# Performance work log

Measured on AMD Instinct MI355X. Metric: run time of the kernel, lower is better.

The kernel has to match this reference:

```python
import jax, jax.numpy as jnp
import numpy as np

B, N, P, PL = 8, 16, 128, 16
D, DS, DTR, DFF, EL = 128, 16, 8, 256, 2


def setup_inputs() -> dict:
    key = jax.random.key(0)
    ks = jax.random.split(key, 16)
    g = lambda i, shape, s=0.02: jax.random.normal(ks[i], shape, dtype=jnp.float32) * s
    A_init = jnp.broadcast_to(jnp.log(jnp.arange(1, DS + 1, dtype=jnp.float32)), (EL, 2, D, DS))
    return dict(
        x=jax.random.normal(ks[0], (B, N, P, PL), dtype=jnp.float32),
        view=jax.random.normal(ks[1], (B, 1, D), dtype=jnp.float32),
        wp_w=g(2, (D, PL)), wp_b=jnp.zeros((D,), jnp.float32),
        m_in_w=g(3, (EL, 2, 2 * D, D)),
        m_conv_w=g(4, (EL, 2, D, 2), 0.5), m_conv_b=jnp.zeros((EL, 2, D), jnp.float32),
        m_xproj_w=g(5, (EL, 2, DTR + 2 * DS, D)),
        m_dt_w=g(6, (EL, 2, D, DTR), 0.1), m_dt_b=jnp.full((EL, 2, D), -4.6, jnp.float32),
        m_Alog=jnp.array(A_init),
        m_D=jnp.ones((EL, 2, D), jnp.float32),
        m_out_w=g(7, (EL, 2, D, D)),
        ffn_w1=g(8, (EL, DFF, D)), ffn_b1=jnp.zeros((EL, DFF), jnp.float32),
        ffn_w2=g(9, (EL, D, DFF)), ffn_b2=jnp.zeros((EL, D), jnp.float32),
        ln1_g=jnp.ones((EL, D), jnp.float32), ln1_b=jnp.zeros((EL, D), jnp.float32),
        ln2_g=jnp.ones((EL, D), jnp.float32), ln2_b=jnp.zeros((EL, D), jnp.float32),
        lnf_g=jnp.ones((D,), jnp.float32), lnf_b=jnp.zeros((D,), jnp.float32),
    )


def _ln(x, g, b, eps=1e-5):
    m = x.mean(-1, keepdims=True)
    v = x.var(-1, keepdims=True)
    return (x - m) * jax.lax.rsqrt(v + eps) * g + b


def _mamba(u, in_w, conv_w, conv_b, xproj_w, dt_w, dt_b, A_log, Dp, out_w):
    # u: [b, L, d]; d_inner == d_model (expand=1), causal depthwise conv with kernel 2
    dtr, ds = dt_w.shape[1], A_log.shape[1]
    xz = u @ in_w.T                               # [b, L, 2d]
    xc, z = jnp.split(xz, 2, axis=-1)
    xp = jnp.pad(xc, ((0, 0), (1, 0), (0, 0)))    # left-pad (d_conv-1 = 1)
    xc = xp[:, :-1, :] * conv_w[:, 0] + xp[:, 1:, :] * conv_w[:, 1] + conv_b
    xc = jax.nn.silu(xc)
    dbc = xc @ xproj_w.T                          # [b, L, dtr + 2*ds]
    dt = jax.nn.softplus(dbc[..., :dtr] @ dt_w.T + dt_b)   # [b, L, d]
    Bm = dbc[..., dtr:dtr + ds]                   # [b, L, n]
    Cm = dbc[..., dtr + ds:]                      # [b, L, n]
    A = -jnp.exp(A_log)                           # [d, n]
    dA = jnp.exp(dt[..., None] * A)               # [b, L, d, n]
    dBx = dt[..., None] * Bm[:, :, None, :] * xc[..., None]  # [b, L, d, n]

    def step(h, ab):
        a, bx = ab
        h = a * h + bx
        return h, h

    h0 = jnp.zeros((u.shape[0], dt.shape[-1], ds), u.dtype)
    _, hs = jax.lax.scan(step, h0, (jnp.moveaxis(dA, 1, 0), jnp.moveaxis(dBx, 1, 0)))
    y = jnp.einsum('lbdn,bln->bld', hs, Cm)       # [b, L, d]
    y = y + xc * Dp
    y = y * jax.nn.silu(z)
    return y @ out_w.T


def _layer(u, pf, pr, w1, b1, w2, b2, g1, be1, g2, be2):
    fwd = _mamba(u, *pf)
    rev = _mamba(u[:, ::-1], *pr)[:, ::-1]
    u = u + fwd + rev
    xr = _ln(u, g1, be1)
    y = jax.nn.relu(xr @ w1.T + b1) @ w2.T + b2   # 1x1 conv FFN == pointwise linear
    return _ln(xr + y, g2, be2)


def reference(x, view, wp_w, wp_b, m_in_w, m_conv_w, m_conv_b, m_xproj_w, m_dt_w,
              m_dt_b, m_Alog, m_D, m_out_w, ffn_w1, ffn_b1, ffn_w2, ffn_b2,
              ln1_g, ln1_b, ln2_g, ln2_b, lnf_g, lnf_b):
    b, n, p, _ = x.shape
    u = x @ wp_w.T + wp_b                         # [b, n, p, d]
    d = u.shape[-1]
    u = u.reshape(b, n * p, d)
    u = jnp.concatenate([u, view], axis=1)        # [b, n*p+1, d]
    for l in range(m_in_w.shape[0]):
        pf = (m_in_w[l, 0], m_conv_w[l, 0], m_conv_b[l, 0], m_xproj_w[l, 0],
              m_dt_w[l, 0], m_dt_b[l, 0], m_Alog[l, 0], m_D[l, 0], m_out_w[l, 0])
        pr = (m_in_w[l, 1], m_conv_w[l, 1], m_conv_b[l, 1], m_xproj_w[l, 1],
              m_dt_w[l, 1], m_dt_b[l, 1], m_Alog[l, 1], m_D[l, 1], m_out_w[l, 1])
        u = _layer(u, pf, pr, ffn_w1[l], ffn_b1[l], ffn_w2[l], ffn_b2[l],
                   ln1_g[l], ln1_b[l], ln2_g[l], ln2_b[l])
    u = _ln(u, lnf_g, lnf_b)
    z = u[:, :-1, :].reshape(b, n, p, d)
    return z.transpose(0, 1, 3, 2)                # [b, n, d, p]
```

## Files before the change

kernel.cpp:

```cpp
#include <hip/hip_runtime.h>
#include <hip/hip_bf16.h>
#include <math.h>

#define DEV __device__ __forceinline__

constexpr int B  = 8,  N = 16, P = 128, PL = 16;
constexpr int D  = 128, DS = 16, DTR = 8, DFF = 256, EL = 2;
constexpr int L  = N * P + 1;
constexpr int BL = B * L;
constexpr int CT = 32;
constexpr int NC = (L + CT - 1) / CT;
constexpr int MT64  = (BL + 63) / 64;
constexpr int MT32  = (BL + 31) / 32;
constexpr int KS = 136;
constexpr int HS = 264;

using bf16x8 = __attribute__((ext_vector_type(8))) __bf16;
using f32x4  = __attribute__((ext_vector_type(4))) float;

DEV float sigmoidf_(float x) { return 1.0f / (1.0f + __expf(-x)); }

DEV void pow_tree(float r, float* pw) {
  float r2 = r * r;
  float r3 = r2 * r;
  float r4 = r2 * r2;
  float r8 = r4 * r4;
  float r12 = r8 * r4;
  pw[0] = r;       pw[1] = r2;      pw[2] = r3;      pw[3] = r4;
  pw[4] = r4 * r;  pw[5] = r4 * r2; pw[6] = r4 * r3; pw[7] = r8;
  pw[8] = r8 * r;  pw[9] = r8 * r2; pw[10] = r8 * r3; pw[11] = r12;
  pw[12] = r12 * r; pw[13] = r12 * r2; pw[14] = r12 * r3; pw[15] = r12 * r4;
}

DEV bool an_is_linear(const float* An) {
  bool ok = true;
#pragma unroll
  for (int n = 0; n < DS; ++n)
    ok = ok && (fabsf(An[n] + (float)(n + 1)) < 1e-3f * (n + 1));
  return ok;
}

__global__ __launch_bounds__(256) void k_prep(
    const float* __restrict__ in_w, const float* __restrict__ conv_w,
    const float* __restrict__ xproj, const float* __restrict__ out_w,
    const float* __restrict__ w1, const float* __restrict__ w2,
    __bf16* __restrict__ weff, __bf16* __restrict__ xpw_bf,
    __bf16* __restrict__ outw_bf, __bf16* __restrict__ w1_bf,
    __bf16* __restrict__ w2_bf)
{
  int g = blockIdx.x * 256 + threadIdx.x;
  if (g < 262144) {
    int l = g >> 17;
    int r = g & 131071;
    int dir = r >> 16;
    int r2 = r & 65535;
    int col = r2 >> 8;
    int kk = r2 & 255;
    int chunk = kk >> 7, k = kk & 127;
    int ld = l * 2 + dir;
    float v;
    if (col < 128) {
      v = in_w[((size_t)ld * 256 + col) * 128 + k] *
          conv_w[((size_t)ld * 128 + col) * 2 + chunk];
    } else {
      v = chunk ? in_w[((size_t)ld * 256 + col) * 128 + k] : 0.f;
    }
    weff[((size_t)ld * 256 + col) * 256 + chunk * 128 + k] = (__bf16)v;
    return;
  }
  g -= 262144;
  if (g < 20480) { xpw_bf[g] = (__bf16)xproj[g]; return; }
  g -= 20480;
  if (g < 65536) {
    int k = g & 127; int q = g >> 7; int n = q & 127; int q2 = q >> 7;
    int dir = q2 & 1; int l = q2 >> 1;
    outw_bf[((size_t)(l * 128 + n)) * 256 + dir * 128 + k] = (__bf16)out_w[g];
    return;
  }
  g -= 65536;
  if (g < 65536) { w1_bf[g] = (__bf16)w1[g]; return; }
  g -= 65536;
  if (g < 65536) { w2_bf[g] = (__bf16)w2[g]; return; }
}

__global__ __launch_bounds__(256) void k_embed(
    const float* __restrict__ x, const float* __restrict__ view,
    const float* __restrict__ wp_w, const float* __restrict__ wp_b,
    float* __restrict__ U, __bf16* __restrict__ Ubf)
{
  int g = blockIdx.x * 256 + threadIdx.x;
  if (g >= BL * D) return;
  int d = g & (D - 1);
  int row = g >> 7;
  int b = row / L, t = row % L;
  float acc;
  if (t < N * P) {
    const float* xr = x + ((size_t)b * N * P + t) * PL;
    acc = wp_b[d];
#pragma unroll
    for (int k = 0; k < PL; ++k) acc += xr[k] * wp_w[d * PL + k];
  } else {
    acc = view[b * D + d];
  }
  U[(size_t)row * D + d] = acc;
  Ubf[(size_t)row * D + d] = (__bf16)acc;
}

__global__ __launch_bounds__(256) void k_front(
    const __bf16* __restrict__ Ubf, const __bf16* __restrict__ Weff,
    const float* __restrict__ conv_b_l, const __bf16* __restrict__ xpw,
    const float* __restrict__ dt_w_l, const float* __restrict__ dt_b_l,
    __bf16* __restrict__ XCCbf, __bf16* __restrict__ Zbf,
    float* __restrict__ BCb, __bf16* __restrict__ DTbf)
{
  __shared__ short As[64 * KS];
  __shared__ short Ws[64 * KS];
  __shared__ float dbs[64][9];
  int bx = blockIdx.x;
  int rdir = bx / MT64;
  int tile = bx % MT64;
  bool isx = (blockIdx.y == 0);
  int tid = threadIdx.x;
  int m0 = tile * 64;
  const __bf16* Wb = Weff + (size_t)rdir * 256 * 256;
  int wave = tid >> 6, lane = tid & 63, lm = lane & 15, lq = lane >> 4;
  int rr0 = tid >> 4, gcol = tid & 15;

  int aoff[4];
  unsigned vmask = 0, smask = 0;
  int shif = rdir ? 128 : -128;
#pragma unroll
  for (int i = 0; i < 4; ++i) {
    int rr = rr0 + 16 * i;
    int m = m0 + rr;
    aoff[i] = 0;
    if (m < BL) {
      int b = m / L, s = m - b * L;
      int idx1 = rdir ? (L - 1 - s) : s;
      aoff[i] = (b * L + idx1) * 128 + gcol * 8;
      vmask |= 1u << i;
      if (s >= 1) smask |= 1u << i;
    }
  }

  f32x4 zero4 = {0.f, 0.f, 0.f, 0.f};
  f32x4 acc[8];
#pragma unroll
  for (int c = 0; c < 8; ++c) acc[c] = zero4;

  int kc0 = isx ? 0 : 1;
  int colx = isx ? 0 : 128;
  for (int kc = kc0; kc < 2; ++kc) {
    if (kc != kc0) __syncthreads();
#pragma unroll
    for (int i = 0; i < 4; ++i) {
      int rr = rr0 + 16 * i;
      int4 v = make_int4(0, 0, 0, 0);
      bool ok = (vmask >> i) & 1;
      if (kc == 0) ok = ok && ((smask >> i) & 1);
      if (ok) v = *(const int4*)(Ubf + aoff[i] + (kc == 0 ? shif : 0));
      *(int4*)&As[rr * KS + gcol * 8] = v;
    }
    for (int ch = 0; ch < 2; ++ch) {
      if (ch) __syncthreads();
#pragma unroll
      for (int i = 0; i < 4; ++i) {
        int rr = rr0 + 16 * i;
        int4 v = *(const int4*)(Wb + (size_t)(colx + ch * 64 + rr) * 256 + kc * 128 + gcol * 8);
        *(int4*)&Ws[rr * KS + gcol * 8] = v;
      }
      __syncthreads();
      for (int ks = 0; ks < 128; ks += 32) {
        bf16x8 af = *(const bf16x8*)&As[(wave * 16 + lm) * KS + ks + lq * 8];
#pragma unroll
        for (int c = 0; c < 4; ++c) {
          bf16x8 bfr = *(const bf16x8*)&Ws[(c * 16 + lm) * KS + ks + lq * 8];
          acc[ch * 4 + c] = __builtin_amdgcn_mfma_f32_16x16x32_bf16(af, bfr, acc[ch * 4 + c], 0, 0, 0);
        }
      }
    }
  }

  if (!isx) {
#pragma unroll
    for (int cg = 0; cg < 8; ++cg) {
      int col = cg * 16 + lm;
#pragma unroll
      for (int e = 0; e < 4; ++e) {
        int m = m0 + wave * 16 + lq * 4 + e;
        if (m < BL)
          Zbf[((size_t)rdir * BL + m) * 128 + col] = (__bf16)acc[cg][e];
      }
    }
    return;
  }

  __syncthreads();
#pragma unroll
  for (int cg = 0; cg < 8; ++cg) {
    int col = cg * 16 + lm;
    float cb = conv_b_l[rdir * 128 + col];
#pragma unroll
    for (int e = 0; e < 4; ++e) {
      int rl = wave * 16 + lq * 4 + e;
      int m = m0 + rl;
      float v = acc[cg][e] + cb;
      float o = v * sigmoidf_(v);
      __bf16 ob = (__bf16)o;
      if (m < BL) XCCbf[((size_t)rdir * BL + m) * 128 + col] = ob;
      As[rl * KS + col] = (short)__builtin_bit_cast(unsigned short, ob);
    }
  }
#pragma unroll
  for (int i = 0; i < 3; ++i) {
    int rr = rr0 + 16 * i;
    int4 v = make_int4(0, 0, 0, 0);
    if (rr < 40) v = *(const int4*)(xpw + ((size_t)rdir * 40 + rr) * 128 + gcol * 8);
    *(int4*)&Ws[rr * KS + gcol * 8] = v;
  }
  __syncthreads();
  f32x4 acc2[3];
#pragma unroll
  for (int c = 0; c < 3; ++c) acc2[c] = zero4;
  for (int ks = 0; ks < 128; ks += 32) {
    bf16x8 af = *(const bf16x8*)&As[(wave * 16 + lm) * KS + ks + lq * 8];
#pragma unroll
    for (int c = 0; c < 3; ++c) {
      bf16x8 bfr = *(const bf16x8*)&Ws[(c * 16 + lm) * KS + ks + lq * 8];
      acc2[c] = __builtin_amdgcn_mfma_f32_16x16x32_bf16(af, bfr, acc2[c], 0, 0, 0);
    }
  }
#pragma unroll
  for (int c = 0; c < 3; ++c) {
    int col = c * 16 + lm;
#pragma unroll
    for (int e = 0; e < 4; ++e) {
      int rl = wave * 16 + lq * 4 + e;
      int m = m0 + rl;
      float v = acc2[c][e];
      if (col < DTR) dbs[rl][col] = v;
      else if (col < DTR + 2 * DS && m < BL)
        BCb[((size_t)rdir * BL + m) * 32 + (col - DTR)] = v;
    }
  }
  __syncthreads();
  {
    int dloc = tid & 127;
    int rpar = tid >> 7;
    const float* dw = dt_w_l + ((size_t)rdir * 128 + dloc) * 8;
    float dwr[8];
#pragma unroll
    for (int j = 0; j < 8; ++j) dwr[j] = dw[j];
    float db = dt_b_l[rdir * 128 + dloc];
    for (int rr = rpar; rr < 64; rr += 2) {
      int m = m0 + rr;
      if (m >= BL) break;
      float a = db;
#pragma unroll
      for (int j = 0; j < 8; ++j) a = fmaf(dbs[rr][j], dwr[j], a);
      float dtv = (a > 20.f) ? a : log1pf(__expf(a));
      DTbf[((size_t)rdir * BL + m) * 128 + dloc] = (__bf16)dtv;
    }
  }
}

__global__ __launch_bounds__(128) void k_scanA(
    const __bf16* __restrict__ DTbf, const __bf16* __restrict__ XCCbf,
    const float* __restrict__ BCb, const float* __restrict__ Alog_l,
    float* __restrict__ HC, float* __restrict__ DTS)
{
  __shared__ float Bs[CT][DS];
  __shared__ __bf16 DTs[CT][128];
  __shared__ __bf16 XCs[CT][128];
  __shared__ float HT[128][DS + 1];
  int blk = blockIdx.x;
  int c  = blk % NC;
  int rb = blk / NC;
  int rdir = rb / B;
  int d = threadIdx.x;
  int s0 = c * CT;
  int cn = min(CT, L - s0);
  size_t rowbase = (size_t)rb * L + s0;
  for (int q = d; q < cn * DS; q += 128)
    Bs[q >> 4][q & 15] = BCb[(rowbase + (q >> 4)) * 32 + (q & 15)];
  for (int q = d; q < cn * 16; q += 128) {
    int row = q >> 4, c8 = (q & 15) * 8;
    *(int4*)&DTs[row][c8] = *(const int4*)(DTbf + (rowbase + row) * D + c8);
    *(int4*)&XCs[row][c8] = *(const int4*)(XCCbf + (rowbase + row) * D + c8);
  }
  float An[DS];
  const float* Ab = Alog_l + (size_t)rdir * D * DS + (size_t)d * DS;
#pragma unroll
  for (int n = 0; n < DS; ++n) An[n] = -__expf(Ab[n]);
  bool fast = an_is_linear(An);
  __syncthreads();
  float h[DS];
#pragma unroll
  for (int n = 0; n < DS; ++n) h[n] = 0.f;
  float dts = 0.f;
  if (fast) {
    for (int ss = 0; ss < cn; ++ss) {
      float dt = (float)DTs[ss][d];
      float xc = (float)XCs[ss][d];
      dts += dt;
      float e = dt * xc;
      float pw[DS];
      pow_tree(__expf(-dt), pw);
#pragma unroll
      for (int n = 0; n < DS; ++n)
        h[n] = fmaf(pw[n], h[n], e * Bs[ss][n]);
    }
  } else {
    for (int ss = 0; ss < cn; ++ss) {
      float dt = (float)DTs[ss][d];
      float xc = (float)XCs[ss][d];
      dts += dt;
      float e = dt * xc;
#pragma unroll
      for (int n = 0; n < DS; ++n)
        h[n] = __expf(dt * An[n]) * h[n] + e * Bs[ss][n];
    }
  }
  DTS[(size_t)blk * D + d] = dts;
#pragma unroll
  for (int n = 0; n < DS; ++n) HT[d][n] = h[n];
  __syncthreads();
  for (int q = d; q < D * DS; q += 128) {
    int n = q >> 7, dd = q & 127;
    HC[((size_t)blk * DS + n) * D + dd] = HT[dd][n];
  }
}

__global__ __launch_bounds__(128) void k_scanB(
    const float* __restrict__ HC, const float* __restrict__ DTS,
    const float* __restrict__ Alog_l, float* __restrict__ HIN)
{
  int rb = blockIdx.x >> 4;
  int n  = blockIdx.x & 15;
  int rdir = rb / B;
  int d = threadIdx.x;
  float An_v = -__expf(Alog_l[((size_t)rdir * D + d) * DS + n]);
  float hc[8], dts[8];
#pragma unroll
  for (int k = 0; k < 8; ++k) {
    int cc = (k < NC) ? k : NC - 1;
    hc[k]  = HC[((size_t)(rb * NC + cc) * DS + n) * D + d];
    dts[k] = DTS[((size_t)(rb * NC + cc)) * D + d];
  }
  float h = 0.f;
  for (int c = 0; c < NC; c += 8) {
#pragma unroll
    for (int k = 0; k < 8; ++k) {
      int cc = c + k;
      if (cc >= NC) break;
      HIN[((size_t)(rb * NC + cc) * DS + n) * D + d] = h;
      h = __expf(dts[k] * An_v) * h + hc[k];
      int cp = cc + 8 < NC ? cc + 8 : NC - 1;
      hc[k]  = HC[((size_t)(rb * NC + cp) * DS + n) * D + d];
      dts[k] = DTS[((size_t)(rb * NC + cp)) * D + d];
    }
  }
}

__global__ __launch_bounds__(128) void k_scanC(
    const __bf16* __restrict__ DTbf, const __bf16* __restrict__ XCCbf,
    const float* __restrict__ BCb, const __bf16* __restrict__ Zbf,
    const float* __restrict__ HIN, const float* __restrict__ Alog_l,
    const float* __restrict__ Dp_l, __bf16* __restrict__ YMbf)
{
  __shared__ float Bsm[CT][DS];
  __shared__ float Csm[CT][DS];
  __shared__ __bf16 DTs[CT][128];
  __shared__ __bf16 XCs[CT][128];
  __shared__ __bf16 Zs[CT][128];
  int blk = blockIdx.x;
  int c  = blk % NC;
  int rb = blk / NC;
  int rdir = rb / B;
  int b = rb % B;
  int d = threadIdx.x;
  int s0 = c * CT;
  int cn = min(CT, L - s0);
  size_t rowbase = (size_t)rb * L + s0;
  for (int q = d; q < cn * 2 * DS; q += 128) {
    int ss = q >> 5, j = q & 31;
    float vv = BCb[(rowbase + ss) * 32 + j];
    if (j < DS) Bsm[ss][j] = vv; else Csm[ss][j - DS] = vv;
  }
  for (int q = d; q < cn * 16; q += 128) {
    int row = q >> 4, c8 = (q & 15) * 8;
    *(int4*)&DTs[row][c8] = *(const int4*)(DTbf + (rowbase + row) * D + c8);
    *(int4*)&XCs[row][c8] = *(const int4*)(XCCbf + (rowbase + row) * D + c8);
    *(int4*)&Zs[row][c8]  = *(const int4*)(Zbf + (rowbase + row) * D + c8);
  }
  float An[DS];
  const float* Ab = Alog_l + (size_t)rdir * D * DS + (size_t)d * DS;
#pragma unroll
  for (int n = 0; n < DS; ++n) An[n] = -__expf(Ab[n]);
  bool fast = an_is_linear(An);
  float h[DS];
#pragma unroll
  for (int n = 0; n < DS; ++n)
    h[n] = HIN[((size_t)blk * DS + n) * D + d];
  float Dpv = Dp_l[rdir * D + d];
  __syncthreads();
  if (fast) {
    for (int ss = 0; ss < cn; ++ss) {
      float dt = (float)DTs[ss][d];
      float xc = (float)XCs[ss][d];
      float z  = (float)Zs[ss][d];
      float e = dt * xc;
      float pw[DS];
      pow_tree(__expf(-dt), pw);
      float y = xc * Dpv;
#pragma unroll
      for (int n = 0; n < DS; ++n) {
        h[n] = fmaf(pw[n], h[n], e * Bsm[ss][n]);
        y = fmaf(h[n], Csm[ss][n], y);
      }
      y *= z * sigmoidf_(z);
      int s = s0 + ss;
      int tt = rdir ? (L - 1 - s) : s;
      YMbf[((size_t)b * L + tt) * 256 + rdir * 128 + d] = (__bf16)y;
    }
  } else {
    for (int ss = 0; ss < cn; ++ss) {
      float dt = (float)DTs[ss][d];
      float xc = (float)XCs[ss][d];
      float z  = (float)Zs[ss][d];
      float e = dt * xc;
      float y = xc * Dpv;
#pragma unroll
      for (int n = 0; n < DS; ++n) {
        h[n] = __expf(dt * An[n]) * h[n] + e * Bsm[ss][n];
        y = fmaf(h[n], Csm[ss][n], y);
      }
      y *= z * sigmoidf_(z);
      int s = s0 + ss;
      int tt = rdir ? (L - 1 - s) : s;
      YMbf[((size_t)b * L + tt) * 256 + rdir * 128 + d] = (__bf16)y;
    }
  }
}

__global__ __launch_bounds__(256) void k_tail(
    const __bf16* __restrict__ YMbf, const __bf16* __restrict__ Wout,
    const float* __restrict__ g1, const float* __restrict__ be1,
    const __bf16* __restrict__ w1bf, const float* __restrict__ b1,
    const __bf16* __restrict__ w2bf, const float* __restrict__ b2,
    const float* __restrict__ g2, const float* __restrict__ be2,
    float* __restrict__ U, __bf16* __restrict__ Ubf,
    int last, const float* __restrict__ lnfg, const float* __restrict__ lnfb,
    float* __restrict__ outp)
{
  __shared__ short AX[32 * KS];
  __shared__ short HB[32 * HS];
  __shared__ short Ws[128 * KS];
  __shared__ float red[2][32][2];
  int m0 = blockIdx.x * 32;
  int tid = threadIdx.x;
  int wave = tid >> 6, lane = tid & 63, lm = lane & 15, lq = lane >> 4;
  int wm = wave >> 1, wn = wave & 1;
  f32x4 zero4 = {0.f, 0.f, 0.f, 0.f};

  f32x4 acc[4];
#pragma unroll
  for (int c = 0; c < 4; ++c) acc[c] = zero4;
  for (int kc = 0; kc < 2; ++kc) {
    if (kc) __syncthreads();
    for (int q = tid; q < 32 * 16; q += 256) {
      int rr = q >> 4, g = q & 15;
      int m = m0 + rr;
      int4 v = make_int4(0, 0, 0, 0);
      if (m < BL) v = *(const int4*)(YMbf + (size_t)m * 256 + kc * 128 + g * 8);
      *(int4*)&AX[rr * KS + g * 8] = v;
    }
    for (int q = tid; q < 128 * 16; q += 256) {
      int rr = q >> 4, g = q & 15;
      int4 v = *(const int4*)(Wout + (size_t)rr * 256 + kc * 128 + g * 8);
      *(int4*)&Ws[rr * KS + g * 8] = v;
    }
    __syncthreads();
    for (int ks = 0; ks < 128; ks += 32) {
      bf16x8 af = *(const bf16x8*)&AX[(wm * 16 + lm) * KS + ks + lq * 8];
#pragma unroll
      for (int c = 0; c < 4; ++c) {
        bf16x8 bfr = *(const bf16x8*)&Ws[(wn * 64 + c * 16 + lm) * KS + ks + lq * 8];
        acc[c] = __builtin_amdgcn_mfma_f32_16x16x32_bf16(af, bfr, acc[c], 0, 0, 0);
      }
    }
  }
  __syncthreads();

  {
    float g1c[4], be1c[4];
#pragma unroll
    for (int c = 0; c < 4; ++c) {
      int col = wn * 64 + c * 16 + lm;
      g1c[c] = g1[col]; be1c[c] = be1[col];
    }
    float os[4][4];
    float mean[4];
#pragma unroll
    for (int r = 0; r < 4; ++r) {
      int rl = wm * 16 + lq * 4 + r;
      int row = m0 + rl;
      bool valid = row < BL;
      float s = 0.f;
#pragma unroll
      for (int c = 0; c < 4; ++c) {
        int col = wn * 64 + c * 16 + lm;
        float uv = valid ? U[(size_t)row * 128 + col] : 0.f;
        os[r][c] = acc[c][r] + uv;
        s += os[r][c];
      }
#pragma unroll
      for (int mm = 1; mm < 16; mm <<= 1) s += __shfl_xor(s, mm, 64);
      if (lm == 0) red[0][rl][wn] = s;
    }
    __syncthreads();
#pragma unroll
    for (int r = 0; r < 4; ++r) {
      int rl = wm * 16 + lq * 4 + r;
      mean[r] = (red[0][rl][0] + red[0][rl][1]) * (1.f / 128.f);
      float qv = 0.f;
#pragma unroll
      for (int c = 0; c < 4; ++c) { float dv = os[r][c] - mean[r]; qv += dv * dv; }
#pragma unroll
      for (int mm = 1; mm < 16; mm <<= 1) qv += __shfl_xor(qv, mm, 64);
      if (lm == 0) red[1][rl][wn] = qv;
    }
    __syncthreads();
#pragma unroll
    for (int r = 0; r < 4; ++r) {
      int rl = wm * 16 + lq * 4 + r;
      float inv = rsqrtf((red[1][rl][0] + red[1][rl][1]) * (1.f / 128.f) + 1e-5f);
#pragma unroll
      for (int c = 0; c < 4; ++c) {
        int col = wn * 64 + c * 16 + lm;
        float o = (os[r][c] - mean[r]) * inv * g1c[c] + be1c[c];
        AX[rl * KS + col] = (short)__builtin_bit_cast(unsigned short, (__bf16)o);
      }
    }
  }

  for (int t = 0; t < 2; ++t) {
    if (t) __syncthreads();
    for (int q = tid; q < 128 * 16; q += 256) {
      int rr = q >> 4, g = q & 15;
      int4 v = *(const int4*)(w1bf + (size_t)(t * 128 + rr) * 128 + g * 8);
      *(int4*)&Ws[rr * KS + g * 8] = v;
    }
    __syncthreads();
    f32x4 a1[4];
#pragma unroll
    for (int c = 0; c < 4; ++c) a1[c] = zero4;
    for (int ks = 0; ks < 128; ks += 32) {
      bf16x8 af = *(const bf16x8*)&AX[(wm * 16 + lm) * KS + ks + lq * 8];
#pragma unroll
      for (int c = 0; c < 4; ++c) {
        bf16x8 bfr = *(const bf16x8*)&Ws[(wn * 64 + c * 16 + lm) * KS + ks + lq * 8];
        a1[c] = __builtin_amdgcn_mfma_f32_16x16x32_bf16(af, bfr, a1[c], 0, 0, 0);
      }
    }
#pragma unroll
    for (int c = 0; c < 4; ++c) {
      int col = t * 128 + wn * 64 + c * 16 + lm;
      float bb = b1[col];
#pragma unroll
      for (int e = 0; e < 4; ++e) {
        int rl = wm * 16 + lq * 4 + e;
        float hv = fmaxf(a1[c][e] + bb, 0.f);
        HB[rl * HS + col] = (short)__builtin_bit_cast(unsigned short, (__bf16)hv);
      }
    }
  }

  f32x4 a2[4];
#pragma unroll
  for (int c = 0; c < 4; ++c) a2[c] = zero4;
  for (int kc = 0; kc < 2; ++kc) {
    __syncthreads();
    for (int q = tid; q < 128 * 16; q += 256) {
      int rr = q >> 4, g = q & 15;
      int4 v = *(const int4*)(w2bf + (size_t)rr * 256 + kc * 128 + g * 8);
      *(int4*)&Ws[rr * KS + g * 8] = v;
    }
    __syncthreads();
    for (int ks = 0; ks < 128; ks += 32) {
      bf16x8 af = *(const bf16x8*)&HB[(wm * 16 + lm) * HS + kc * 128 + ks + lq * 8];
#pragma unroll
      for (int c = 0; c < 4; ++c) {
        bf16x8 bfr = *(const bf16x8*)&Ws[(wn * 64 + c * 16 + lm) * KS + ks + lq * 8];
        a2[c] = __builtin_amdgcn_mfma_f32_16x16x32_bf16(af, bfr, a2[c], 0, 0, 0);
      }
    }
  }
  __syncthreads();

  {
    float b2c[4], g2c[4], be2c[4];
#pragma unroll
    for (int c = 0; c < 4; ++c) {
      int col = wn * 64 + c * 16 + lm;
      b2c[c] = b2[col]; g2c[c] = g2[col]; be2c[c] = be2[col];
    }
    float os[4][4];
    float mean[4];
#pragma unroll
    for (int r = 0; r < 4; ++r) {
      int rl = wm * 16 + lq * 4 + r;
      float s = 0.f;
#pragma unroll
      for (int c = 0; c < 4; ++c) {
        int col = wn * 64 + c * 16 + lm;
        __bf16 xb = __builtin_bit_cast(__bf16, (unsigned short)AX[rl * KS + col]);
        os[r][c] = a2[c][r] + b2c[c] + (float)xb;
        s += os[r][c];
      }
#pragma unroll
      for (int mm = 1; mm < 16; mm <<= 1) s += __shfl_xor(s, mm, 64);
      if (lm == 0) red[0][rl][wn] = s;
    }
    __syncthreads();
#pragma unroll
    for (int r = 0; r < 4; ++r) {
      int rl = wm * 16 + lq * 4 + r;
      mean[r] = (red[0][rl][0] + red[0][rl][1]) * (1.f / 128.f);
      float qv = 0.f;
#pragma unroll
      for (int c = 0; c < 4; ++c) { float dv = os[r][c] - mean[r]; qv += dv * dv; }
#pragma unroll
      for (int mm = 1; mm < 16; mm <<= 1) qv += __shfl_xor(qv, mm, 64);
      if (lm == 0) red[1][rl][wn] = qv;
    }
    __syncthreads();
    float o[4][4];
#pragma unroll
    for (int r = 0; r < 4; ++r) {
      int rl = wm * 16 + lq * 4 + r;
      float inv = rsqrtf((red[1][rl][0] + red[1][rl][1]) * (1.f / 128.f) + 1e-5f);
#pragma unroll
      for (int c = 0; c < 4; ++c)
        o[r][c] = (os[r][c] - mean[r]) * inv * g2c[c] + be2c[c];
    }
    if (!last) {
#pragma unroll
      for (int r = 0; r < 4; ++r) {
        int rl = wm * 16 + lq * 4 + r;
        int row = m0 + rl;
        if (row < BL) {
#pragma unroll
          for (int c = 0; c < 4; ++c) {
            int col = wn * 64 + c * 16 + lm;
            U[(size_t)row * 128 + col] = o[r][c];
          }
        }
#pragma unroll
        for (int c = 0; c < 4; ++c) {
          int col = wn * 64 + c * 16 + lm;
          AX[rl * KS + col] = (short)__builtin_bit_cast(unsigned short, (__bf16)o[r][c]);
        }
      }
    } else {
      float m2[4];
#pragma unroll
      for (int r = 0; r < 4; ++r) {
        int rl = wm * 16 + lq * 4 + r;
        float s2 = 0.f;
#pragma unroll
        for (int c = 0; c < 4; ++c) s2 += o[r][c];
#pragma unroll
        for (int mm = 1; mm < 16; mm <<= 1) s2 += __shfl_xor(s2, mm, 64);
        if (lm == 0) red[0][rl][wn] = s2;
      }
      __syncthreads();
#pragma unroll
      for (int r = 0; r < 4; ++r) {
        int rl = wm * 16 + lq * 4 + r;
        m2[r] = (red[0][rl][0] + red[0][rl][1]) * (1.f / 128.f);
        float q2 = 0.f;
#pragma unroll
        for (int c = 0; c < 4; ++c) { float dv = o[r][c] - m2[r]; q2 += dv * dv; }
#pragma unroll
        for (int mm = 1; mm < 16; mm <<= 1) q2 += __shfl_xor(q2, mm, 64);
        if (lm == 0) red[1][rl][wn] = q2;
      }
      __syncthreads();
#pragma unroll
      for (int r = 0; r < 4; ++r) {
        int rl = wm * 16 + lq * 4 + r;
        int row = m0 + rl;
        float i2 = rsqrtf((red[1][rl][0] + red[1][rl][1]) * (1.f / 128.f) + 1e-5f);
        if (row < BL) {
          int bb = row / L;
          int t = row - bb * L;
          if (t < N * P) {
            int n = t >> 7, p = t & 127;
            size_t obase = (((size_t)bb * N + n) * D) * P + p;
#pragma unroll
            for (int c = 0; c < 4; ++c) {
              int col = wn * 64 + c * 16 + lm;
              float o2 = (o[r][c] - m2[r]) * i2 * lnfg[col] + lnfb[col];
              outp[obase + (size_t)col * P] = o2;
            }
          }
        }
      }
    }
  }
  if (!last) {
    __syncthreads();
    int rr0 = tid >> 4, gcol = tid & 15;
#pragma unroll
    for (int i = 0; i < 2; ++i) {
      int rr = rr0 + 16 * i;
      int m = m0 + rr;
      if (m < BL)
        *(int4*)(Ubf + (size_t)m * 128 + gcol * 8) = *(const int4*)&AX[rr * KS + gcol * 8];
    }
  }
}

extern "C" void kernel_launch(void* const* d_in, const int* in_sizes, int n_in,
                              void* d_out, int out_size, void* d_ws, size_t ws_size,
                              hipStream_t stream)
{
  (void)in_sizes; (void)n_in; (void)out_size; (void)ws_size;
  const float* x       = (const float*)d_in[0];
  const float* view    = (const float*)d_in[1];
  const float* wp_w    = (const float*)d_in[2];
  const float* wp_b    = (const float*)d_in[3];
  const float* m_in_w  = (const float*)d_in[4];
  const float* m_conv_w= (const float*)d_in[5];
  const float* m_conv_b= (const float*)d_in[6];
  const float* m_xproj = (const float*)d_in[7];
  const float* m_dt_w  = (const float*)d_in[8];
  const float* m_dt_b  = (const float*)d_in[9];
  const float* m_Alog  = (const float*)d_in[10];
  const float* m_Dp    = (const float*)d_in[11];
  const float* m_out_w = (const float*)d_in[12];
  const float* ffn_w1  = (const float*)d_in[13];
  const float* ffn_b1  = (const float*)d_in[14];
  const float* ffn_w2  = (const float*)d_in[15];
  const float* ffn_b2  = (const float*)d_in[16];
  const float* ln1_g   = (const float*)d_in[17];
  const float* ln1_b   = (const float*)d_in[18];
  const float* ln2_g   = (const float*)d_in[19];
  const float* ln2_b   = (const float*)d_in[20];
  const float* lnf_g   = (const float*)d_in[21];
  const float* lnf_b   = (const float*)d_in[22];
  float* out = (float*)d_out;

  float* W = (float*)d_ws;
  size_t off = 0;
  auto alloc = [&](size_t nfl) { float* p = W + off; off += (nfl + 3) & ~(size_t)3; return p; };
  float* U      = alloc((size_t)BL * D);
  float* Ubf_f  = alloc((size_t)BL * D / 2);
  float* XCC_f  = alloc((size_t)BL * D);
  float* Zbf_f  = alloc((size_t)BL * D);
  float* DT_f   = alloc((size_t)BL * D);
  float* BCb    = alloc((size_t)2 * BL * 2 * DS);
  float* YM_f   = alloc((size_t)BL * 256 / 2);
  float* HC     = alloc((size_t)2 * B * NC * D * DS);
  float* DTS    = alloc((size_t)2 * B * NC * D);
  float* HIN    = alloc((size_t)2 * B * NC * D * DS);
  float* weff_f = alloc(262144 / 2);
  float* xpw_f  = alloc(20480 / 2);
  float* outw_f = alloc(65536 / 2);
  float* w1_f   = alloc(65536 / 2);
  float* w2_f   = alloc(65536 / 2);

  __bf16* Ubf    = (__bf16*)Ubf_f;
  __bf16* XCCbf  = (__bf16*)XCC_f;
  __bf16* Zbf    = (__bf16*)Zbf_f;
  __bf16* DTbf   = (__bf16*)DT_f;
  __bf16* YMbf   = (__bf16*)YM_f;
  __bf16* weff   = (__bf16*)weff_f;
  __bf16* xpw_bf = (__bf16*)xpw_f;
  __bf16* outw_bf= (__bf16*)outw_f;
  __bf16* w1_bf  = (__bf16*)w1_f;
  __bf16* w2_bf  = (__bf16*)w2_f;

  k_prep<<<1872, 256, 0, stream>>>(m_in_w, m_conv_w, m_xproj, m_out_w, ffn_w1, ffn_w2,
                                   weff, xpw_bf, outw_bf, w1_bf, w2_bf);
  k_embed<<<(BL * D + 255) / 256, 256, 0, stream>>>(x, view, wp_w, wp_b, U, Ubf);

  for (int l = 0; l < EL; ++l) {
    const float* conv_b_l = m_conv_b + (size_t)l * 2 * D;
    const float* dt_w_l   = m_dt_w   + (size_t)l * 2 * D * DTR;
    const float* dt_b_l   = m_dt_b   + (size_t)l * 2 * D;
    const float* Alog_l   = m_Alog   + (size_t)l * 2 * D * DS;
    const float* Dp_l     = m_Dp     + (size_t)l * 2 * D;

    k_front <<<dim3(2 * MT64, 2), 256, 0, stream>>>(
        Ubf, weff + (size_t)l * 2 * 256 * 256, conv_b_l,
        xpw_bf + (size_t)l * 2 * 40 * 128, dt_w_l, dt_b_l,
        XCCbf, Zbf, BCb, DTbf);
    k_scanA <<<2 * B * NC, 128, 0, stream>>>(DTbf, XCCbf, BCb, Alog_l, HC, DTS);
    k_scanB <<<2 * B * 16, 128, 0, stream>>>(HC, DTS, Alog_l, HIN);
    k_scanC <<<2 * B * NC, 128, 0, stream>>>(DTbf, XCCbf, BCb, Zbf, HIN, Alog_l, Dp_l, YMbf);
    k_tail  <<<MT32, 256, 0, stream>>>(
        YMbf, outw_bf + (size_t)l * 128 * 256,
        ln1_g + l * D, ln1_b + l * D,
        w1_bf + (size_t)l * 256 * 128, ffn_b1 + l * DFF,
        w2_bf + (size_t)l * 128 * 256, ffn_b2 + l * D,
        ln2_g + l * D, ln2_b + l * D, U, Ubf,
        (l == EL - 1) ? 1 : 0, lnf_g, lnf_b, out);
  }
}
```

Measured before the change: 339.9 us.

## Merge prep/embed kernels, prefetch GEMM tiles into registers, simplify scan stores

Merges the weight-prep and embedding kernels into one launch. In k_front and k_tail, weight and activation tiles (and the residual U values) are now loaded into registers up front or one stage ahead, so global-load latency overlaps with MFMA work. The scan kernels issue all global loads before computing A and store to shared memory afterward. k_scanA writes HC straight from registers instead of transposing through a shared tile, and softplus uses __logf(1+exp) instead of log1pf. The cost is much higher register pressure, which may lower occupancy, plus slightly less accurate softplus for very negative inputs.

```diff
diff --git a/kernel.cpp b/kernel.cpp
--- a/kernel.cpp
+++ b/kernel.cpp
@@ -14,6 +14,8 @@
 constexpr int MT32  = (BL + 31) / 32;
 constexpr int KS = 136;
 constexpr int HS = 264;
+constexpr int PREP_BLOCKS  = 1872;
+constexpr int EMBED_BLOCKS = (BL * D + 255) / 256;
 
 using bf16x8 = __attribute__((ext_vector_type(8))) __bf16;
 using f32x4  = __attribute__((ext_vector_type(4))) float;
@@ -40,55 +42,55 @@
   return ok;
 }
 
-__global__ __launch_bounds__(256) void k_prep(
+__global__ __launch_bounds__(256) void k_init(
     const float* __restrict__ in_w, const float* __restrict__ conv_w,
     const float* __restrict__ xproj, const float* __restrict__ out_w,
     const float* __restrict__ w1, const float* __restrict__ w2,
     __bf16* __restrict__ weff, __bf16* __restrict__ xpw_bf,
     __bf16* __restrict__ outw_bf, __bf16* __restrict__ w1_bf,
-    __bf16* __restrict__ w2_bf)
-{
-  int g = blockIdx.x * 256 + threadIdx.x;
-  if (g < 262144) {
-    int l = g >> 17;
-    int r = g & 131071;
-    int dir = r >> 16;
-    int r2 = r & 65535;
-    int col = r2 >> 8;
-    int kk = r2 & 255;
-    int chunk = kk >> 7, k = kk & 127;
-    int ld = l * 2 + dir;
-    float v;
-    if (col < 128) {
-      v = in_w[((size_t)ld * 256 + col) * 128 + k] *
-          conv_w[((size_t)ld * 128 + col) * 2 + chunk];
-    } else {
-      v = chunk ? in_w[((size_t)ld * 256 + col) * 128 + k] : 0.f;
-    }
-    weff[((size_t)ld * 256 + col) * 256 + chunk * 128 + k] = (__bf16)v;
-    return;
-  }
-  g -= 262144;
-  if (g < 20480) { xpw_bf[g] = (__bf16)xproj[g]; return; }
-  g -= 20480;
-  if (g < 65536) {
-    int k = g & 127; int q = g >> 7; int n = q & 127; int q2 = q >> 7;
-    int dir = q2 & 1; int l = q2 >> 1;
-    outw_bf[((size_t)(l * 128 + n)) * 256 + dir * 128 + k] = (__bf16)out_w[g];
-    return;
-  }
-  g -= 65536;
-  if (g < 65536) { w1_bf[g] = (__bf16)w1[g]; return; }
-  g -= 65536;
-  if (g < 65536) { w2_bf[g] = (__bf16)w2[g]; return; }
-}
-
-__global__ __launch_bounds__(256) void k_embed(
+    __bf16* __restrict__ w2_bf,
     const float* __restrict__ x, const float* __restrict__ view,
     const float* __restrict__ wp_w, const float* __restrict__ wp_b,
     float* __restrict__ U, __bf16* __restrict__ Ubf)
 {
-  int g = blockIdx.x * 256 + threadIdx.x;
+  int bid = blockIdx.x;
+  if (bid < PREP_BLOCKS) {
+    int g = bid * 256 + threadIdx.x;
+    if (g < 262144) {
+      int l = g >> 17;
+      int r = g & 131071;
+      int dir = r >> 16;
+      int r2 = r & 65535;
+      int col = r2 >> 8;
+      int kk = r2 & 255;
+      int chunk = kk >> 7, k = kk & 127;
+      int ld = l * 2 + dir;
+      float v;
+      if (col < 128) {
+        v = in_w[((size_t)ld * 256 + col) * 128 + k] *
+            conv_w[((size_t)ld * 128 + col) * 2 + chunk];
+      } else {
+        v = chunk ? in_w[((size_t)ld * 256 + col) * 128 + k] : 0.f;
+      }
+      weff[((size_t)ld * 256 + col) * 256 + chunk * 128 + k] = (__bf16)v;
+      return;
+    }
+    g -= 262144;
+    if (g < 20480) { xpw_bf[g] = (__bf16)xproj[g]; return; }
+    g -= 20480;
+    if (g < 65536) {
+      int k = g & 127; int q = g >> 7; int n = q & 127; int q2 = q >> 7;
+      int dir = q2 & 1; int l = q2 >> 1;
+      outw_bf[((size_t)(l * 128 + n)) * 256 + dir * 128 + k] = (__bf16)out_w[g];
+      return;
+    }
+    g -= 65536;
+    if (g < 65536) { w1_bf[g] = (__bf16)w1[g]; return; }
+    g -= 65536;
+    if (g < 65536) { w2_bf[g] = (__bf16)w2[g]; return; }
+    return;
+  }
+  int g = (bid - PREP_BLOCKS) * 256 + threadIdx.x;
   if (g >= BL * D) return;
   int d = g & (D - 1);
   int row = g >> 7;
@@ -125,6 +127,24 @@
   const __bf16* Wb = Weff + (size_t)rdir * 256 * 256;
   int wave = tid >> 6, lane = tid & 63, lm = lane & 15, lq = lane >> 4;
   int rr0 = tid >> 4, gcol = tid & 15;
+  int kc0 = isx ? 0 : 1;
+  int colx = isx ? 0 : 128;
+
+  int4 wpA[4], wpB[4], wpC[4], wpD[4];
+#pragma unroll
+  for (int j = 0; j < 4; ++j)
+    wpA[j] = *(const int4*)(Wb + (size_t)(colx + 0 * 64 + rr0 + 16 * j) * 256 + kc0 * 128 + gcol * 8);
+#pragma unroll
+  for (int j = 0; j < 4; ++j)
+    wpB[j] = *(const int4*)(Wb + (size_t)(colx + 1 * 64 + rr0 + 16 * j) * 256 + kc0 * 128 + gcol * 8);
+  if (isx) {
+#pragma unroll
+    for (int j = 0; j < 4; ++j)
+      wpC[j] = *(const int4*)(Wb + (size_t)(colx + 0 * 64 + rr0 + 16 * j) * 256 + 128 + gcol * 8);
+#pragma unroll
+    for (int j = 0; j < 4; ++j)
+      wpD[j] = *(const int4*)(Wb + (size_t)(colx + 1 * 64 + rr0 + 16 * j) * 256 + 128 + gcol * 8);
+  }
 
   int aoff[4];
   unsigned vmask = 0, smask = 0;
@@ -148,26 +168,30 @@
 #pragma unroll
   for (int c = 0; c < 8; ++c) acc[c] = zero4;
 
-  int kc0 = isx ? 0 : 1;
-  int colx = isx ? 0 : 128;
   for (int kc = kc0; kc < 2; ++kc) {
     if (kc != kc0) __syncthreads();
-#pragma unroll
-    for (int i = 0; i < 4; ++i) {
-      int rr = rr0 + 16 * i;
-      int4 v = make_int4(0, 0, 0, 0);
-      bool ok = (vmask >> i) & 1;
-      if (kc == 0) ok = ok && ((smask >> i) & 1);
-      if (ok) v = *(const int4*)(Ubf + aoff[i] + (kc == 0 ? shif : 0));
-      *(int4*)&As[rr * KS + gcol * 8] = v;
+    {
+      int4 av[4];
+#pragma unroll
+      for (int i = 0; i < 4; ++i) {
+        av[i] = make_int4(0, 0, 0, 0);
+        bool ok = (vmask >> i) & 1;
+        if (kc == 0) ok = ok && ((smask >> i) & 1);
+        if (ok) av[i] = *(const int4*)(Ubf + aoff[i] + (kc == 0 ? shif : 0));
+      }
+#pragma unroll
+      for (int i = 0; i < 4; ++i)
+        *(int4*)&As[(rr0 + 16 * i) * KS + gcol * 8] = av[i];
     }
     for (int ch = 0; ch < 2; ++ch) {
       if (ch) __syncthreads();
-#pragma unroll
-      for (int i = 0; i < 4; ++i) {
-        int rr = rr0 + 16 * i;
-        int4 v = *(const int4*)(Wb + (size_t)(colx + ch * 64 + rr) * 256 + kc * 128 + gcol * 8);
-        *(int4*)&Ws[rr * KS + gcol * 8] = v;
+      {
+        int pidx = (kc - kc0) * 2 + ch;
+#pragma unroll
+        for (int i = 0; i < 4; ++i) {
+          int4 wv = (pidx == 0) ? wpA[i] : (pidx == 1) ? wpB[i] : (pidx == 2) ? wpC[i] : wpD[i];
+          *(int4*)&Ws[(rr0 + 16 * i) * KS + gcol * 8] = wv;
+        }
       }
       __syncthreads();
       for (int ks = 0; ks < 128; ks += 32) {
@@ -211,12 +235,17 @@
       As[rl * KS + col] = (short)__builtin_bit_cast(unsigned short, ob);
     }
   }
-#pragma unroll
-  for (int i = 0; i < 3; ++i) {
-    int rr = rr0 + 16 * i;
-    int4 v = make_int4(0, 0, 0, 0);
-    if (rr < 40) v = *(const int4*)(xpw + ((size_t)rdir * 40 + rr) * 128 + gcol * 8);
-    *(int4*)&Ws[rr * KS + gcol * 8] = v;
+  {
+    int4 xv[3];
+#pragma unroll
+    for (int i = 0; i < 3; ++i) {
+      int rr = rr0 + 16 * i;
+      xv[i] = make_int4(0, 0, 0, 0);
+      if (rr < 40) xv[i] = *(const int4*)(xpw + ((size_t)rdir * 40 + rr) * 128 + gcol * 8);
+    }
+#pragma unroll
+    for (int i = 0; i < 3; ++i)
+      *(int4*)&Ws[(rr0 + 16 * i) * KS + gcol * 8] = xv[i];
   }
   __syncthreads();
   f32x4 acc2[3];
@@ -258,7 +287,7 @@
       float a = db;
 #pragma unroll
       for (int j = 0; j < 8; ++j) a = fmaf(dbs[rr][j], dwr[j], a);
-      float dtv = (a > 20.f) ? a : log1pf(__expf(a));
+      float dtv = (a > 20.f) ? a : __logf(1.f + __expf(a));
       DTbf[((size_t)rdir * BL + m) * 128 + dloc] = (__bf16)dtv;
     }
   }
@@ -272,7 +301,6 @@
   __shared__ float Bs[CT][DS];
   __shared__ __bf16 DTs[CT][128];
   __shared__ __bf16 XCs[CT][128];
-  __shared__ float HT[128][DS + 1];
   int blk = blockIdx.x;
   int c  = blk % NC;
   int rb = blk / NC;
@@ -281,18 +309,48 @@
   int s0 = c * CT;
   int cn = min(CT, L - s0);
   size_t rowbase = (size_t)rb * L + s0;
-  for (int q = d; q < cn * DS; q += 128)
-    Bs[q >> 4][q & 15] = BCb[(rowbase + (q >> 4)) * 32 + (q & 15)];
-  for (int q = d; q < cn * 16; q += 128) {
+
+  int totB = cn * DS;
+  float bb[4]; bool bp[4];
+#pragma unroll
+  for (int i = 0; i < 4; ++i) {
+    int q = d + i * 128;
+    bp[i] = q < totB;
+    bb[i] = bp[i] ? BCb[(rowbase + (q >> 4)) * 32 + (q & 15)] : 0.f;
+  }
+  int totD = cn * 16;
+  int4 dv[4], xv[4]; bool dp[4];
+#pragma unroll
+  for (int i = 0; i < 4; ++i) {
+    int q = d + i * 128;
+    dp[i] = q < totD;
+    dv[i] = make_int4(0, 0, 0, 0);
+    xv[i] = make_int4(0, 0, 0, 0);
     int row = q >> 4, c8 = (q & 15) * 8;
-    *(int4*)&DTs[row][c8] = *(const int4*)(DTbf + (rowbase + row) * D + c8);
-    *(int4*)&XCs[row][c8] = *(const int4*)(XCCbf + (rowbase + row) * D + c8);
+    if (dp[i]) {
+      dv[i] = *(const int4*)(DTbf + (rowbase + row) * D + c8);
+      xv[i] = *(const int4*)(XCCbf + (rowbase + row) * D + c8);
+    }
   }
   float An[DS];
   const float* Ab = Alog_l + (size_t)rdir * D * DS + (size_t)d * DS;
 #pragma unroll
   for (int n = 0; n < DS; ++n) An[n] = -__expf(Ab[n]);
   bool fast = an_is_linear(An);
+#pragma unroll
+  for (int i = 0; i < 4; ++i) {
+    int q = d + i * 128;
+    if (bp[i]) Bs[q >> 4][q & 15] = bb[i];
+  }
+#pragma unroll
+  for (int i = 0; i < 4; ++i) {
+    int q = d + i * 128;
+    int row = q >> 4, c8 = (q & 15) * 8;
+    if (dp[i]) {
+      *(int4*)&DTs[row][c8] = dv[i];
+      *(int4*)&XCs[row][c8] = xv[i];
+    }
+  }
   __syncthreads();
   float h[DS];
 #pragma unroll
@@ -323,12 +381,8 @@
   }
   DTS[(size_t)blk * D + d] = dts;
 #pragma unroll
-  for (int n = 0; n < DS; ++n) HT[d][n] = h[n];
-  __syncthreads();
-  for (int q = d; q < D * DS; q += 128) {
-    int n = q >> 7, dd = q & 127;
-    HC[((size_t)blk * DS + n) * D + dd] = HT[dd][n];
-  }
+  for (int n = 0; n < DS; ++n)
+    HC[((size_t)blk * DS + n) * D + d] = h[n];
 }
 
 __global__ __launch_bounds__(128) void k_scanB(
@@ -382,16 +436,30 @@
   int s0 = c * CT;
   int cn = min(CT, L - s0);
   size_t rowbase = (size_t)rb * L + s0;
-  for (int q = d; q < cn * 2 * DS; q += 128) {
-    int ss = q >> 5, j = q & 31;
-    float vv = BCb[(rowbase + ss) * 32 + j];
-    if (j < DS) Bsm[ss][j] = vv; else Csm[ss][j - DS] = vv;
-  }
-  for (int q = d; q < cn * 16; q += 128) {
+
+  int tot2 = cn * 2 * DS;
+  float cbv[8]; bool cbp[8];
+#pragma unroll
+  for (int i = 0; i < 8; ++i) {
+    int q = d + i * 128;
+    cbp[i] = q < tot2;
+    cbv[i] = cbp[i] ? BCb[(rowbase + (q >> 5)) * 32 + (q & 31)] : 0.f;
+  }
+  int totD = cn * 16;
+  int4 dv[4], xv[4], zv[4]; bool dp[4];
+#pragma unroll
+  for (int i = 0; i < 4; ++i) {
+    int q = d + i * 128;
+    dp[i] = q < totD;
+    dv[i] = make_int4(0, 0, 0, 0);
+    xv[i] = make_int4(0, 0, 0, 0);
+    zv[i] = make_int4(0, 0, 0, 0);
     int row = q >> 4, c8 = (q & 15) * 8;
-    *(int4*)&DTs[row][c8] = *(const int4*)(DTbf + (rowbase + row) * D + c8);
-    *(int4*)&XCs[row][c8] = *(const int4*)(XCCbf + (rowbase + row) * D + c8);
-    *(int4*)&Zs[row][c8]  = *(const int4*)(Zbf + (rowbase + row) * D + c8);
+    if (dp[i]) {
+      dv[i] = *(const int4*)(DTbf + (rowbase + row) * D + c8);
+      xv[i] = *(const int4*)(XCCbf + (rowbase + row) * D + c8);
+      zv[i] = *(const int4*)(Zbf + (rowbase + row) * D + c8);
+    }
   }
   float An[DS];
   const float* Ab = Alog_l + (size_t)rdir * D * DS + (size_t)d * DS;
@@ -403,6 +471,24 @@
   for (int n = 0; n < DS; ++n)
     h[n] = HIN[((size_t)blk * DS + n) * D + d];
   float Dpv = Dp_l[rdir * D + d];
+#pragma unroll
+  for (int i = 0; i < 8; ++i) {
+    int q = d + i * 128;
+    if (cbp[i]) {
+      int ss = q >> 5, j = q & 31;
+      if (j < DS) Bsm[ss][j] = cbv[i]; else Csm[ss][j - DS] = cbv[i];
+    }
+  }
+#pragma unroll
+  for (int i = 0; i < 4; ++i) {
+    int q = d + i * 128;
+    int row = q >> 4, c8 = (q & 15) * 8;
+    if (dp[i]) {
+      *(int4*)&DTs[row][c8] = dv[i];
+      *(int4*)&XCs[row][c8] = xv[i];
+      *(int4*)&Zs[row][c8]  = zv[i];
+    }
+  }
   __syncthreads();
   if (fast) {
     for (int ss = 0; ss < cn; ++ss) {
@@ -461,24 +547,61 @@
   int tid = threadIdx.x;
   int wave = tid >> 6, lane = tid & 63, lm = lane & 15, lq = lane >> 4;
   int wm = wave >> 1, wn = wave & 1;
+  int rr0 = tid >> 4, gcol = tid & 15;
   f32x4 zero4 = {0.f, 0.f, 0.f, 0.f};
 
+  int4 ym0[2], ym1[2], wo0[8], wo1[8];
+#pragma unroll
+  for (int j = 0; j < 2; ++j) {
+    int m = m0 + rr0 + j * 16;
+    ym0[j] = make_int4(0, 0, 0, 0);
+    if (m < BL) ym0[j] = *(const int4*)(YMbf + (size_t)m * 256 + gcol * 8);
+  }
+#pragma unroll
+  for (int j = 0; j < 8; ++j)
+    wo0[j] = *(const int4*)(Wout + (size_t)(rr0 + j * 16) * 256 + gcol * 8);
+#pragma unroll
+  for (int j = 0; j < 2; ++j) {
+    int m = m0 + rr0 + j * 16;
+    ym1[j] = make_int4(0, 0, 0, 0);
+    if (m < BL) ym1[j] = *(const int4*)(YMbf + (size_t)m * 256 + 128 + gcol * 8);
+  }
+#pragma unroll
+  for (int j = 0; j < 8; ++j)
+    wo1[j] = *(const int4*)(Wout + (size_t)(rr0 + j * 16) * 256 + 128 + gcol * 8);
+
+  float uvp[4][4];
+#pragma unroll
+  for (int r = 0; r < 4; ++r) {
+    int row = m0 + wm * 16 + lq * 4 + r;
+    bool valid = row < BL;
+#pragma unroll
+    for (int c = 0; c < 4; ++c) {
+      int col = wn * 64 + c * 16 + lm;
+      uvp[r][c] = valid ? U[(size_t)row * 128 + col] : 0.f;
+    }
+  }
+
+  int4 w1t0[8], w1t1[8];
   f32x4 acc[4];
 #pragma unroll
   for (int c = 0; c < 4; ++c) acc[c] = zero4;
+#pragma unroll
   for (int kc = 0; kc < 2; ++kc) {
     if (kc) __syncthreads();
-    for (int q = tid; q < 32 * 16; q += 256) {
-      int rr = q >> 4, g = q & 15;
-      int m = m0 + rr;
-      int4 v = make_int4(0, 0, 0, 0);
-      if (m < BL) v = *(const int4*)(YMbf + (size_t)m * 256 + kc * 128 + g * 8);
-      *(int4*)&AX[rr * KS + g * 8] = v;
-    }
-    for (int q = tid; q < 128 * 16; q += 256) {
-      int rr = q >> 4, g = q & 15;
-      int4 v = *(const int4*)(Wout + (size_t)rr * 256 + kc * 128 + g * 8);
-      *(int4*)&Ws[rr * KS + g * 8] = v;
+#pragma unroll
+    for (int j = 0; j < 2; ++j)
+      *(int4*)&AX[(rr0 + j * 16) * KS + gcol * 8] = kc ? ym1[j] : ym0[j];
+#pragma unroll
+    for (int j = 0; j < 8; ++j)
+      *(int4*)&Ws[(rr0 + j * 16) * KS + gcol * 8] = kc ? wo1[j] : wo0[j];
+    if (kc == 1) {
+#pragma unroll
+      for (int j = 0; j < 8; ++j)
+        w1t0[j] = *(const int4*)(w1bf + (size_t)(0 * 128 + rr0 + j * 16) * 128 + gcol * 8);
+#pragma unroll
+      for (int j = 0; j < 8; ++j)
+        w1t1[j] = *(const int4*)(w1bf + (size_t)(1 * 128 + rr0 + j * 16) * 128 + gcol * 8);
     }
     __syncthreads();
     for (int ks = 0; ks < 128; ks += 32) {
@@ -504,14 +627,10 @@
 #pragma unroll
     for (int r = 0; r < 4; ++r) {
       int rl = wm * 16 + lq * 4 + r;
-      int row = m0 + rl;
-      bool valid = row < BL;
       float s = 0.f;
 #pragma unroll
       for (int c = 0; c < 4; ++c) {
-        int col = wn * 64 + c * 16 + lm;
-        float uv = valid ? U[(size_t)row * 128 + col] : 0.f;
-        os[r][c] = acc[c][r] + uv;
+        os[r][c] = acc[c][r] + uvp[r][c];
         s += os[r][c];
       }
 #pragma unroll
@@ -544,12 +663,20 @@
     }
   }
 
+  int4 w2k0[8], w2k1[8];
+#pragma unroll
   for (int t = 0; t < 2; ++t) {
     if (t) __syncthreads();
-    for (int q = tid; q < 128 * 16; q += 256) {
-      int rr = q >> 4, g = q & 15;
-      int4 v = *(const int4*)(w1bf + (size_t)(t * 128 + rr) * 128 + g * 8);
-      *(int4*)&Ws[rr * KS + g * 8] = v;
+#pragma unroll
+    for (int j = 0; j < 8; ++j)
+      *(int4*)&Ws[(rr0 + j * 16) * KS + gcol * 8] = t ? w1t1[j] : w1t0[j];
+    if (t == 1) {
+#pragma unroll
+      for (int j = 0; j < 8; ++j)
+        w2k0[j] = *(const int4*)(w2bf + (size_t)(rr0 + j * 16) * 256 + gcol * 8);
+#pragma unroll
+      for (int j = 0; j < 8; ++j)
+        w2k1[j] = *(const int4*)(w2bf + (size_t)(rr0 + j * 16) * 256 + 128 + gcol * 8);
     }
     __syncthreads();
     f32x4 a1[4];
@@ -579,13 +706,12 @@
   f32x4 a2[4];
 #pragma unroll
   for (int c = 0; c < 4; ++c) a2[c] = zero4;
+#pragma unroll
   for (int kc = 0; kc < 2; ++kc) {
     __syncthreads();
-    for (int q = tid; q < 128 * 16; q += 256) {
-      int rr = q >> 4, g = q & 15;
-      int4 v = *(const int4*)(w2bf + (size_t)rr * 256 + kc * 128 + g * 8);
-      *(int4*)&Ws[rr * KS + g * 8] = v;
-    }
+#pragma unroll
+    for (int j = 0; j < 8; ++j)
+      *(int4*)&Ws[(rr0 + j * 16) * KS + gcol * 8] = kc ? w2k1[j] : w2k0[j];
     __syncthreads();
     for (int ks = 0; ks < 128; ks += 32) {
       bf16x8 af = *(const bf16x8*)&HB[(wm * 16 + lm) * HS + kc * 128 + ks + lq * 8];
@@ -711,7 +837,6 @@
   }
   if (!last) {
     __syncthreads();
-    int rr0 = tid >> 4, gcol = tid & 15;
 #pragma unroll
     for (int i = 0; i < 2; ++i) {
       int rr = rr0 + 16 * i;
@@ -782,9 +907,10 @@
   __bf16* w1_bf  = (__bf16*)w1_f;
   __bf16* w2_bf  = (__bf16*)w2_f;
 
-  k_prep<<<1872, 256, 0, stream>>>(m_in_w, m_conv_w, m_xproj, m_out_w, ffn_w1, ffn_w2,
-                                   weff, xpw_bf, outw_bf, w1_bf, w2_bf);
-  k_embed<<<(BL * D + 255) / 256, 256, 0, stream>>>(x, view, wp_w, wp_b, U, Ubf);
+  k_init<<<PREP_BLOCKS + EMBED_BLOCKS, 256, 0, stream>>>(
+      m_in_w, m_conv_w, m_xproj, m_out_w, ffn_w1, ffn_w2,
+      weff, xpw_bf, outw_bf, w1_bf, w2_bf,
+      x, view, wp_w, wp_b, U, Ubf);
 
   for (int l = 0; l < EL; ++l) {
     const float* conv_b_l = m_conv_b + (size_t)l * 2 * D;
```

Result: slower. 349.0 us (+2.7%).
